# Kernel tuning notes

Measured on AMD Instinct MI355X. Metric: run time of the kernel, lower is better.

## Reference

```python
import jax, jax.numpy as jnp
import numpy as np

EPS = 0.01  # softening length (use_softening=True)


def setup_inputs() -> dict:
    key = jax.random.key(0)
    ks = jax.random.split(key, 4)
    B, N, H = 2, 2048, 64
    s1 = 1.0 / np.sqrt(2.0)
    s2 = 1.0 / np.sqrt(H)
    return {
        "pos": jax.random.normal(ks[0], (B, N, 3), dtype=jnp.float32),
        "W1": jax.random.normal(ks[1], (2, H), dtype=jnp.float32) * s1,
        "b1": jnp.zeros((H,), dtype=jnp.float32),
        "W2": jax.random.normal(ks[2], (H, H), dtype=jnp.float32) * s2,
        "b2": jnp.zeros((H,), dtype=jnp.float32),
        "W3": jax.random.normal(ks[3], (H, 1), dtype=jnp.float32) * s2,
        "b3": jnp.zeros((1,), dtype=jnp.float32),
    }


def reference(pos, W1, b1, W2, b2, W3, b3):
    B, N, _ = pos.shape
    # Static upper-triangular pair indices (E = N(N-1)/2)
    i_idx, j_idx = jnp.triu_indices(N, k=1)

    # Pairwise displacement vectors: [B, E, 3]
    r_ij = pos[:, j_idx, :] - pos[:, i_idx, :]

    dist_sq = jnp.sum(r_ij * r_ij, axis=-1, keepdims=True) + EPS * EPS  # [B, E, 1]
    dist = jnp.sqrt(dist_sq)
    inv_dist_cube = 1.0 / (dist_sq * dist)
    edge_features = jnp.concatenate([dist, inv_dist_cube], axis=-1)  # [B, E, 2]

    # Small 3-layer MLP on edge features -> scalar message m_ij
    h = jax.nn.relu(edge_features @ W1 + b1)
    h = jax.nn.relu(h @ W2 + b2)
    m_ij = h @ W3 + b3  # [B, E, 1]

    f_ij = m_ij * r_ij  # [B, E, 3]

    # Scatter-add forces (Newton's third law: +f to i, -f to j)
    acc = jnp.zeros_like(pos)
    acc = acc.at[:, i_idx, :].add(f_ij)
    acc = acc.at[:, j_idx, :].add(-f_ij)
    return acc
```

## Files before the change

kernel.cpp:

```cpp
#include <hip/hip_runtime.h>


#define EPS2      1.0e-4f
#define TAB_BITS  6
#define TAB_SHIFT (23 - TAB_BITS)
#define TAB_EMIN  113
#define TAB_BASE  (TAB_EMIN << TAB_BITS)
#define TAB_OCT   22
#define TAB_N     (TAB_OCT << TAB_BITS)

#define NPART  2048
#define BLOCK  512
#define CHUNK  512
#define NSPLIT 64
#define JPT    (NPART / NSPLIT)

__global__ void build_table(const float* __restrict__ W1, const float* __restrict__ b1,
                            const float* __restrict__ W2, const float* __restrict__ b2,
                            const float* __restrict__ W3, const float* __restrict__ b3,
                            float* __restrict__ tab, float* __restrict__ out, int out_n) {
    const int t = blockIdx.x * blockDim.x + threadIdx.x;

    if (t < out_n) out[t] = 0.0f;

    const int entry = t >> 6;
    const int o     = t & 63;
    if (entry > TAB_N) return;

    const unsigned u = (unsigned)(entry + TAB_BASE) << TAB_SHIFT;
    const float s = __uint_as_float(u);
    const float d = sqrtf(s);
    const float idc = 1.0f / (s * d);

    float acc = b2[o];
#pragma unroll
    for (int k = 0; k < 64; ++k) {
        float hv = fmaf(d, W1[k], fmaf(idc, W1[64 + k], b1[k]));
        hv = hv > 0.0f ? hv : 0.0f;
        acc = fmaf(hv, W2[k * 64 + o], acc);
    }
    float part = (acc > 0.0f ? acc : 0.0f) * W3[o];

    part += __shfl_down(part, 32, 64);
    part += __shfl_down(part, 16, 64);
    part += __shfl_down(part, 8, 64);
    part += __shfl_down(part, 4, 64);
    part += __shfl_down(part, 2, 64);
    part += __shfl_down(part, 1, 64);
    if (o == 0) tab[entry] = part + b3[0];
}

__global__ __launch_bounds__(BLOCK, 4)
void forces(const float* __restrict__ pos, const float* __restrict__ tab,
            float* __restrict__ out) {
    __shared__ float2 tabs[TAB_N + 1];

    const int tid = threadIdx.x;

    for (int k = tid; k < TAB_N; k += BLOCK) {
        float t0 = tab[k], t1 = tab[k + 1];
        float s0 = __uint_as_float((unsigned)(k + TAB_BASE) << TAB_SHIFT);
        float rcpw = __uint_as_float((unsigned)(147 - (k >> TAB_BITS)) << 23);
        float a = (t1 - t0) * rcpw;
        tabs[k] = make_float2(a, fmaf(-a, s0, t0));
    }
    __syncthreads();

    const int split = blockIdx.x;
    const int chunk = blockIdx.y;
    const int b     = blockIdx.z;

    const float* posb = pos + (size_t)b * NPART * 3;
    const int i = chunk * CHUNK + tid;
    const float pix = posb[i * 3 + 0];
    const float piy = posb[i * 3 + 1];
    const float piz = posb[i * 3 + 2];

    float ax = 0.0f, ay = 0.0f, az = 0.0f;
    const float* pj = posb + split * JPT * 3;

#pragma unroll 8
    for (int jj = 0; jj < JPT; ++jj) {
        float dx = pj[jj * 3 + 0] - pix;
        float dy = pj[jj * 3 + 1] - piy;
        float dz = pj[jj * 3 + 2] - piz;
        float s = fmaf(dx, dx, fmaf(dy, dy, fmaf(dz, dz, EPS2)));
        unsigned idx = (__float_as_uint(s) >> TAB_SHIFT) - TAB_BASE;
        idx = idx > TAB_N - 1u ? TAB_N - 1u : idx;
        float2 ab = tabs[idx];
        float m = fmaf(s, ab.x, ab.y);
        ax = fmaf(m, dx, ax);
        ay = fmaf(m, dy, ay);
        az = fmaf(m, dz, az);
    }

    float* o = out + ((size_t)b * NPART + i) * 3;
    atomicAdd(o + 0, ax);
    atomicAdd(o + 1, ay);
    atomicAdd(o + 2, az);
}

extern "C" void kernel_launch(void* const* d_in, const int* in_sizes, int n_in,
                              void* d_out, int out_size, void* d_ws, size_t ws_size,
                              hipStream_t stream) {
    const float* pos = (const float*)d_in[0];
    const float* W1  = (const float*)d_in[1];
    const float* b1  = (const float*)d_in[2];
    const float* W2  = (const float*)d_in[3];
    const float* b2  = (const float*)d_in[4];
    const float* W3  = (const float*)d_in[5];
    const float* b3  = (const float*)d_in[6];
    float* out = (float*)d_out;
    float* tab = (float*)d_ws;

    const int B = in_sizes[0] / (NPART * 3);

    const int build_threads = (TAB_N + 1) * 64;
    build_table<<<(build_threads + 255) / 256, 256, 0, stream>>>(
        W1, b1, W2, b2, W3, b3, tab, out, out_size);

    forces<<<dim3(NSPLIT, NPART / CHUNK, B), BLOCK, 0, stream>>>(pos, tab, out);
}
```

Baseline: 83.16 us.

## Reduce forces in-block with shuffles and shared memory instead of global atomics

Each block now owns 16 target particles and splits the source loop across 32 thread groups. Partial forces are combined with wave shuffles and a shared-memory pass, then written directly. This removes the global atomic adds and the output zeroing in the table kernel. The trade-offs are half as many blocks, each with twice the per-thread work, and non-uniform position loads within a wave.

```diff
diff --git a/kernel.cpp b/kernel.cpp
--- a/kernel.cpp
+++ b/kernel.cpp
@@ -11,18 +11,15 @@
 
 #define NPART  2048
 #define BLOCK  512
-#define CHUNK  512
-#define NSPLIT 64
-#define JPT    (NPART / NSPLIT)
+#define WI     16
+#define NSPL   (BLOCK / WI)
+#define JPT    (NPART / NSPL)
 
 __global__ void build_table(const float* __restrict__ W1, const float* __restrict__ b1,
                             const float* __restrict__ W2, const float* __restrict__ b2,
                             const float* __restrict__ W3, const float* __restrict__ b3,
-                            float* __restrict__ tab, float* __restrict__ out, int out_n) {
+                            float* __restrict__ tab) {
     const int t = blockIdx.x * blockDim.x + threadIdx.x;
-
-    if (t < out_n) out[t] = 0.0f;
-
     const int entry = t >> 6;
     const int o     = t & 63;
     if (entry > TAB_N) return;
@@ -54,6 +51,7 @@
 void forces(const float* __restrict__ pos, const float* __restrict__ tab,
             float* __restrict__ out) {
     __shared__ float2 tabs[TAB_N + 1];
+    __shared__ float red[BLOCK / 64][WI][3];
 
     const int tid = threadIdx.x;
 
@@ -66,18 +64,19 @@
     }
     __syncthreads();
 
-    const int split = blockIdx.x;
-    const int chunk = blockIdx.y;
-    const int b     = blockIdx.z;
+    const int bx = blockIdx.x;
+    const int b  = blockIdx.y;
+    const int il = tid & (WI - 1);
+    const int sp = tid >> 4;
+    const int i  = bx * WI + il;
 
     const float* posb = pos + (size_t)b * NPART * 3;
-    const int i = chunk * CHUNK + tid;
     const float pix = posb[i * 3 + 0];
     const float piy = posb[i * 3 + 1];
     const float piz = posb[i * 3 + 2];
 
     float ax = 0.0f, ay = 0.0f, az = 0.0f;
-    const float* pj = posb + split * JPT * 3;
+    const float* pj = posb + sp * JPT * 3;
 
 #pragma unroll 8
     for (int jj = 0; jj < JPT; ++jj) {
@@ -94,10 +93,27 @@
         az = fmaf(m, dz, az);
     }
 
-    float* o = out + ((size_t)b * NPART + i) * 3;
-    atomicAdd(o + 0, ax);
-    atomicAdd(o + 1, ay);
-    atomicAdd(o + 2, az);
+    ax += __shfl_xor(ax, 16, 64); ax += __shfl_xor(ax, 32, 64);
+    ay += __shfl_xor(ay, 16, 64); ay += __shfl_xor(ay, 32, 64);
+    az += __shfl_xor(az, 16, 64); az += __shfl_xor(az, 32, 64);
+
+    const int lane = tid & 63;
+    const int w    = tid >> 6;
+    if (lane < WI) {
+        red[w][lane][0] = ax;
+        red[w][lane][1] = ay;
+        red[w][lane][2] = az;
+    }
+    __syncthreads();
+
+    if (tid < WI * 3) {
+        const int ii = tid / 3;
+        const int c  = tid - ii * 3;
+        float sum = 0.0f;
+#pragma unroll
+        for (int w2 = 0; w2 < BLOCK / 64; ++w2) sum += red[w2][ii][c];
+        out[((size_t)b * NPART + bx * WI + ii) * 3 + c] = sum;
+    }
 }
 
 extern "C" void kernel_launch(void* const* d_in, const int* in_sizes, int n_in,
@@ -117,7 +133,7 @@
 
     const int build_threads = (TAB_N + 1) * 64;
     build_table<<<(build_threads + 255) / 256, 256, 0, stream>>>(
-        W1, b1, W2, b2, W3, b3, tab, out, out_size);
+        W1, b1, W2, b2, W3, b3, tab);
 
-    forces<<<dim3(NSPLIT, NPART / CHUNK, B), BLOCK, 0, stream>>>(pos, tab, out);
+    forces<<<dim3(NPART / WI, B), BLOCK, 0, stream>>>(pos, tab, out);
 }
```

New measurement: 74.79 us. 10.1% less time.
